# Performance work log

Measured on AMD Instinct MI355X. Metric: run time of the kernel, lower is better.

Reference implementation:

```python
import jax, jax.numpy as jnp
import numpy as np

B, L, D, H = 32, 1024, 512, 512
ODE_STEPS = 6
DT = 1.0

def _unif(key, shape, fan_in):
    bound = 1.0 / np.sqrt(fan_in)
    return jax.random.uniform(key, shape, jnp.float32, -bound, bound)

def setup_inputs() -> dict:
    key = jax.random.key(0)
    ks = jax.random.split(key, 9)
    return {
        "x": jax.random.normal(ks[0], (B, L, D), jnp.float32),
        "log_tau": jnp.zeros((H,), jnp.float32),
        "W_in": _unif(ks[1], (H, D), D),
        "b_in": _unif(ks[2], (H,), D),
        "W_rec": _unif(ks[3], (H, H), H),
        "W_gate": _unif(ks[4], (H, D + H), D + H),
        "b_gate": _unif(ks[5], (H,), D + H),
        "W_out": _unif(ks[6], (H, H), H),
        "b_out": _unif(ks[7], (H,), H),
    }

def reference(x, log_tau, W_in, b_in, W_rec, W_gate, b_gate, W_out, b_out):
    Bx, Lx, Dx = x.shape
    Hx = log_tau.shape[0]
    tau = jnp.exp(log_tau)                      # (H,)
    sub_dt = DT / ODE_STEPS
    # Split gate weight: cat([x, h]) @ W_gate.T == x @ Wg_x.T + h @ Wg_h.T
    Wg_x, Wg_h = W_gate[:, :Dx], W_gate[:, Dx:]
    # Precompute input-dependent drives for the whole sequence (time-parallel GEMMs)
    drive = jnp.einsum('bld,hd->blh', x, W_in) + b_in      # W_in(x), (B,L,H)
    gate_x = jnp.einsum('bld,hd->blh', x, Wg_x) + b_gate   # input part of gate pre-act

    def step(h, inp):
        d, gx = inp  # (B,H) each
        for _ in range(ODE_STEPS):  # small fixed unroll of ODE sub-steps
            rec = h @ W_rec.T
            gate = jax.nn.sigmoid(gx + h @ Wg_h.T)
            f = -h + gate * jnp.tanh(d + rec)
            h = h + (sub_dt / tau) * f
        return h, h

    h0 = jnp.zeros((Bx, Hx), x.dtype)
    h_last, fwd = jax.lax.scan(step, h0, (drive.transpose(1, 0, 2), gate_x.transpose(1, 0, 2)))
    fwd = fwd.transpose(1, 0, 2)                 # (B,L,H)
    output = fwd @ W_out.T + b_out               # output_proj; dropout is identity (p=0)
    return output, h_last
```

## Files before the change

kernel.cpp:

```cpp
#include <hip/hip_runtime.h>

typedef unsigned short u16;
typedef unsigned int   u32;
typedef unsigned long long u64;

#define LTC_B 32
#define LTC_L 1024
#define LTC_D 512
#define LTC_H 512
#define NG 8
#define NP 16
#define NBG 4

typedef _Float16 f16x8  __attribute__((ext_vector_type(8)));
typedef _Float16 f16x2t __attribute__((ext_vector_type(2)));
typedef float    f32x4  __attribute__((ext_vector_type(4)));

static __device__ __forceinline__ u32 packh(float a, float b) {
    f16x2t p; p[0] = (_Float16)a; p[1] = (_Float16)b;
    return __builtin_bit_cast(u32, p);
}
static __device__ __forceinline__ float unplo(u32 w) {
    return (float)__builtin_bit_cast(f16x2t, w)[0];
}
static __device__ __forceinline__ float unphi(u32 w) {
    return (float)__builtin_bit_cast(f16x2t, w)[1];
}
static __device__ __forceinline__ float sigm(float x) {
    return 1.f / (1.f + __expf(-x));
}
static __device__ __forceinline__ float tanh_f(float x) {
    float e = __expf(2.f * x);
    return 1.f - 2.f / (e + 1.f);
}
static __device__ __forceinline__ f16x8 cvt8(const float* p) {
    const float4 a = *(const float4*)p;
    const float4 b = *(const float4*)(p + 4);
    f16x8 r;
    r[0] = (_Float16)a.x; r[1] = (_Float16)a.y; r[2] = (_Float16)a.z; r[3] = (_Float16)a.w;
    r[4] = (_Float16)b.x; r[5] = (_Float16)b.y; r[6] = (_Float16)b.z; r[7] = (_Float16)b.w;
    return r;
}
static __device__ __forceinline__ bool stamp4(u64 a, u64 b, u64 c, u64 d, u32 k) {
    return ((u32)(a >> 32) == k) & ((u32)(b >> 32) == k) &
           ((u32)(c >> 32) == k) & ((u32)(d >> 32) == k);
}

__global__ __launch_bounds__(256) void gemm_a32_c16(
    const float* __restrict__ A, const float* __restrict__ W, int ldb,
    const float* __restrict__ bias, u16* __restrict__ C)
{
    const int wave = threadIdx.x >> 6;
    const int lane = threadIdx.x & 63;
    const int tile = blockIdx.x * 4 + wave;
    const int nt = tile & 7;
    const int mt = tile >> 3;
    const int r16 = lane & 15;
    const int kq  = (lane >> 4) * 8;

    const float* ap = A + (size_t)(mt * 64 + r16) * LTC_D + kq;
    const float* wp = W + (size_t)(nt * 64 + r16) * ldb + kq;

    f32x4 acc[4][4];
    #pragma unroll
    for (int i = 0; i < 4; ++i)
        #pragma unroll
        for (int jj = 0; jj < 4; ++jj) acc[i][jj] = (f32x4){0.f, 0.f, 0.f, 0.f};

    for (int ks = 0; ks < 16; ++ks) {
        f16x8 af[4], bf[4];
        #pragma unroll
        for (int t = 0; t < 4; ++t) {
            af[t] = cvt8(ap + (size_t)t * 16 * LTC_D + ks * 32);
            bf[t] = cvt8(wp + (size_t)t * 16 * ldb  + ks * 32);
        }
        #pragma unroll
        for (int mi = 0; mi < 4; ++mi)
            #pragma unroll
            for (int ni = 0; ni < 4; ++ni)
                acc[mi][ni] = __builtin_amdgcn_mfma_f32_16x16x32_f16(
                    af[mi], bf[ni], acc[mi][ni], 0, 0, 0);
    }
    const int row = (lane >> 4) * 4;
    const int col = lane & 15;
    #pragma unroll
    for (int ni = 0; ni < 4; ++ni) {
        const int n = nt * 64 + ni * 16 + col;
        const float bv = bias[n];
        #pragma unroll
        for (int mi = 0; mi < 4; ++mi)
            #pragma unroll
            for (int r = 0; r < 4; ++r) {
                _Float16 h = (_Float16)(acc[mi][ni][r] + bv);
                C[(size_t)(mt * 64 + mi * 16 + row + r) * LTC_H + n] =
                    __builtin_bit_cast(u16, h);
            }
    }
}

__global__ __launch_bounds__(256) void gemm_a16_c32(
    const u16* __restrict__ A, const float* __restrict__ W,
    const float* __restrict__ bias, float* __restrict__ C)
{
    const int wave = threadIdx.x >> 6;
    const int lane = threadIdx.x & 63;
    const int tile = blockIdx.x * 4 + wave;
    const int nt = tile & 7;
    const int mt = tile >> 3;
    const int r16 = lane & 15;
    const int kq  = (lane >> 4) * 8;

    const _Float16* ap = (const _Float16*)A + (size_t)(mt * 64 + r16) * LTC_D + kq;
    const float*    wp = W + (size_t)(nt * 64 + r16) * LTC_H + kq;

    f32x4 acc[4][4];
    #pragma unroll
    for (int i = 0; i < 4; ++i)
        #pragma unroll
        for (int jj = 0; jj < 4; ++jj) acc[i][jj] = (f32x4){0.f, 0.f, 0.f, 0.f};

    for (int ks = 0; ks < 16; ++ks) {
        f16x8 af[4], bf[4];
        #pragma unroll
        for (int t = 0; t < 4; ++t) {
            af[t] = *(const f16x8*)(ap + (size_t)t * 16 * LTC_D + ks * 32);
            bf[t] = cvt8(wp + (size_t)t * 16 * LTC_H + ks * 32);
        }
        #pragma unroll
        for (int mi = 0; mi < 4; ++mi)
            #pragma unroll
            for (int ni = 0; ni < 4; ++ni)
                acc[mi][ni] = __builtin_amdgcn_mfma_f32_16x16x32_f16(
                    af[mi], bf[ni], acc[mi][ni], 0, 0, 0);
    }
    const int row = (lane >> 4) * 4;
    const int col = lane & 15;
    #pragma unroll
    for (int ni = 0; ni < 4; ++ni) {
        const int n = nt * 64 + ni * 16 + col;
        const float bv = bias[n];
        #pragma unroll
        for (int mi = 0; mi < 4; ++mi)
            #pragma unroll
            for (int r = 0; r < 4; ++r)
                C[(size_t)(mt * 64 + mi * 16 + row + r) * LTC_H + n] =
                    acc[mi][ni][r] + bv;
    }
}

__global__ __launch_bounds__(256) void ltc_scan(
    u32* __restrict__ drive,
    const u32* __restrict__ gatex,
    const float* __restrict__ W_rec,
    const float* __restrict__ W_gate,
    const float* __restrict__ log_tau,
    u64* __restrict__ hbuf,
    float* __restrict__ hlast)
{
    const int g   = blockIdx.x & 7;
    const int p   = blockIdx.x >> 3;
    const int tid = threadIdx.x;
    const int lane = tid & 63;
    const int wv   = tid >> 6;

    __shared__ u32 hTu[16][260];
    __shared__ float red[64][17];

    const int nl = wv * 16 + (lane & 15);
    const int kq = (lane >> 4) * 8;
    const float* wrow = (nl < 32)
        ? (W_rec  + (size_t)(32 * p + nl) * LTC_H)
        : (W_gate + (size_t)(32 * p + nl - 32) * (LTC_D + LTC_H) + LTC_D);
    f16x8 Wf[16];
    #pragma unroll
    for (int ks = 0; ks < 16; ++ks) Wf[ks] = cvt8(wrow + ks * 32 + kq);

    for (int i = tid; i < 16 * 260; i += 256) (&hTu[0][0])[i] = 0;
    __syncthreads();

    const int ub = tid >> 4;
    const int jp = tid & 15;
    const int j0 = 32 * p + 2 * jp;
    const int gb = g * NBG + ub;
    float h0 = 0.f, h1 = 0.f, stau0 = 0.f, stau1 = 0.f;
    size_t dwofs = 0;
    if (tid < 64) {
        stau0 = (1.f / 6.f) * __expf(-log_tau[j0]);
        stau1 = (1.f / 6.f) * __expf(-log_tau[j0 + 1]);
        dwofs = (size_t)gb * LTC_L * 256 + 16 * p + jp;
    }

    const _Float16* hrow = (const _Float16*)&hTu[lane & 15][0];
    u32 kp1 = 0;
    int budget = 1 << 22;

    u32 dw = 0, gw = 0;
    if (tid < 64) { dw = drive[dwofs]; gw = gatex[dwofs]; }

    for (int l = 0; l < LTC_L; ++l) {
        const float d0 = unplo(dw), d1 = unphi(dw);
        const float gx0 = unplo(gw), gx1 = unphi(gw);
        u32 dn = 0, gn = 0;
        if (tid < 64 && l + 1 < LTC_L) {
            dn = drive[dwofs + (size_t)(l + 1) * 256];
            gn = gatex[dwofs + (size_t)(l + 1) * 256];
        }
        #pragma unroll 1
        for (int s = 0; s < 6; ++s) {
            f32x4 acc0 = (f32x4){0.f, 0.f, 0.f, 0.f}, acc1 = acc0;
            #pragma unroll
            for (int ks = 0; ks < 16; ks += 2) {
                const f16x8 a0 = *(const f16x8*)(hrow + ks * 32 + kq);
                const f16x8 a1 = *(const f16x8*)(hrow + (ks + 1) * 32 + kq);
                acc0 = __builtin_amdgcn_mfma_f32_16x16x32_f16(a0, Wf[ks],     acc0, 0, 0, 0);
                acc1 = __builtin_amdgcn_mfma_f32_16x16x32_f16(a1, Wf[ks + 1], acc1, 0, 0, 0);
            }
            {
                const int n  = wv * 16 + (lane & 15);
                const int rb = (lane >> 4) * 4;
                #pragma unroll
                for (int r = 0; r < 4; ++r) red[n][rb + r] = acc0[r] + acc1[r];
            }
            __syncthreads();
            ++kp1;
            const size_t pbase = (size_t)((kp1 & 1u) * NG + g) * (NBG * 256);
            if (tid < 64) {
                const float rec0 = red[2 * jp][ub],     gh0 = red[32 + 2 * jp][ub];
                const float rec1 = red[2 * jp + 1][ub], gh1 = red[32 + 2 * jp + 1][ub];
                h0 += stau0 * (sigm(gx0 + gh0) * tanh_f(d0 + rec0) - h0);
                h1 += stau1 * (sigm(gx1 + gh1) * tanh_f(d1 + rec1) - h1);
                const u64 v = ((u64)kp1 << 32) | (u64)packh(h0, h1);
                __hip_atomic_store(hbuf + pbase + (size_t)ub * 256 + 16 * p + jp,
                                   v, __ATOMIC_RELAXED, __HIP_MEMORY_SCOPE_AGENT);
            }
            {
                const u64* sb = hbuf + pbase + tid;
                u64 a0, a1, a2, a3;
                bool ok;
                do {
                    a0 = __hip_atomic_load(sb,       __ATOMIC_RELAXED,
                                           __HIP_MEMORY_SCOPE_AGENT);
                    a1 = __hip_atomic_load(sb + 256, __ATOMIC_RELAXED,
                                           __HIP_MEMORY_SCOPE_AGENT);
                    a2 = __hip_atomic_load(sb + 512, __ATOMIC_RELAXED,
                                           __HIP_MEMORY_SCOPE_AGENT);
                    a3 = __hip_atomic_load(sb + 768, __ATOMIC_RELAXED,
                                           __HIP_MEMORY_SCOPE_AGENT);
                    ok = stamp4(a0, a1, a2, a3, kp1);
                } while (!ok && --budget > 0);
                hTu[0][tid] = (u32)a0; hTu[1][tid] = (u32)a1;
                hTu[2][tid] = (u32)a2; hTu[3][tid] = (u32)a3;
            }
            __syncthreads();
        }
        if (tid < 64) drive[dwofs + (size_t)l * 256] = packh(h0, h1);
        dw = dn; gw = gn;
    }
    if (tid < 64) {
        hlast[(size_t)gb * LTC_H + j0]     = h0;
        hlast[(size_t)gb * LTC_H + j0 + 1] = h1;
    }
}

extern "C" void kernel_launch(void* const* d_in, const int* in_sizes, int n_in,
                              void* d_out, int out_size, void* d_ws, size_t ws_size,
                              hipStream_t stream)
{
    const float* x       = (const float*)d_in[0];
    const float* log_tau = (const float*)d_in[1];
    const float* W_in    = (const float*)d_in[2];
    const float* b_in    = (const float*)d_in[3];
    const float* W_rec   = (const float*)d_in[4];
    const float* W_gate  = (const float*)d_in[5];
    const float* b_gate  = (const float*)d_in[6];
    const float* W_out   = (const float*)d_in[7];
    const float* b_out   = (const float*)d_in[8];

    float* out   = (float*)d_out;
    float* hlast = out + (size_t)LTC_B * LTC_L * LTC_H;

    u32* ws    = (u32*)d_ws;
    u32* drive = ws;
    u32* gatex = ws + 8388608;
    u64* hbuf  = (u64*)(ws + 16777216);

    const int blocks = (LTC_B * LTC_L / 64) * (LTC_H / 64) / 4;

    gemm_a32_c16<<<blocks, 256, 0, stream>>>(x, W_in, LTC_D, b_in, (u16*)drive);
    gemm_a32_c16<<<blocks, 256, 0, stream>>>(x, W_gate, LTC_D + LTC_H, b_gate, (u16*)gatex);
    ltc_scan<<<NG * NP, 256, 0, stream>>>(drive, gatex, W_rec, W_gate, log_tau,
                                          hbuf, hlast);
    gemm_a16_c32<<<blocks, 256, 0, stream>>>((const u16*)drive, W_out, b_out, out);
}
```

Measured before the change: 10.81 ms.

## Pipeline recurrent scan per batch-row chunk to overlap polling with MFMA

```diff
diff --git a/kernel.cpp b/kernel.cpp
--- a/kernel.cpp
+++ b/kernel.cpp
@@ -40,10 +40,6 @@
     r[0] = (_Float16)a.x; r[1] = (_Float16)a.y; r[2] = (_Float16)a.z; r[3] = (_Float16)a.w;
     r[4] = (_Float16)b.x; r[5] = (_Float16)b.y; r[6] = (_Float16)b.z; r[7] = (_Float16)b.w;
     return r;
-}
-static __device__ __forceinline__ bool stamp4(u64 a, u64 b, u64 c, u64 d, u32 k) {
-    return ((u32)(a >> 32) == k) & ((u32)(b >> 32) == k) &
-           ((u32)(c >> 32) == k) & ((u32)(d >> 32) == k);
 }
 
 __global__ __launch_bounds__(256) void gemm_a32_c16(
@@ -164,7 +160,7 @@
     const int wv   = tid >> 6;
 
     __shared__ u32 hTu[16][260];
-    __shared__ float red[64][17];
+    __shared__ float redc[4][68];
 
     const int nl = wv * 16 + (lane & 15);
     const int kq = (lane >> 4) * 8;
@@ -207,51 +203,42 @@
         }
         #pragma unroll 1
         for (int s = 0; s < 6; ++s) {
-            f32x4 acc0 = (f32x4){0.f, 0.f, 0.f, 0.f}, acc1 = acc0;
-            #pragma unroll
-            for (int ks = 0; ks < 16; ks += 2) {
-                const f16x8 a0 = *(const f16x8*)(hrow + ks * 32 + kq);
-                const f16x8 a1 = *(const f16x8*)(hrow + (ks + 1) * 32 + kq);
-                acc0 = __builtin_amdgcn_mfma_f32_16x16x32_f16(a0, Wf[ks],     acc0, 0, 0, 0);
-                acc1 = __builtin_amdgcn_mfma_f32_16x16x32_f16(a1, Wf[ks + 1], acc1, 0, 0, 0);
+            ++kp1;
+            const u32 pk = kp1 - 1;
+            const size_t pubbase = (size_t)(((kp1 & 1u) * NG + g) * NBG) * 256;
+            const size_t polbase = (size_t)(((pk  & 1u) * NG + g) * NBG) * 256;
+            #pragma unroll
+            for (int c = 0; c < NBG; ++c) {
+                if (pk) {
+                    const u64* sb = hbuf + polbase + (size_t)c * 256 + tid;
+                    u64 v;
+                    do {
+                        v = __hip_atomic_load(sb, __ATOMIC_RELAXED,
+                                              __HIP_MEMORY_SCOPE_AGENT);
+                    } while ((u32)(v >> 32) != pk && --budget > 0);
+                    hTu[c][tid] = (u32)v;
+                }
+                __syncthreads();
+                f32x4 acc0 = (f32x4){0.f, 0.f, 0.f, 0.f}, acc1 = acc0;
+                #pragma unroll
+                for (int ks = 0; ks < 16; ks += 2) {
+                    const f16x8 a0 = *(const f16x8*)(hrow + ks * 32 + kq);
+                    const f16x8 a1 = *(const f16x8*)(hrow + (ks + 1) * 32 + kq);
+                    acc0 = __builtin_amdgcn_mfma_f32_16x16x32_f16(a0, Wf[ks],     acc0, 0, 0, 0);
+                    acc1 = __builtin_amdgcn_mfma_f32_16x16x32_f16(a1, Wf[ks + 1], acc1, 0, 0, 0);
+                }
+                if (lane < 16) redc[c][wv * 16 + lane] = acc0[c] + acc1[c];
+                __syncthreads();
+                if (tid < 64 && ub == c) {
+                    const float rec0 = redc[c][2 * jp],      gh0 = redc[c][32 + 2 * jp];
+                    const float rec1 = redc[c][2 * jp + 1],  gh1 = redc[c][33 + 2 * jp];
+                    h0 += stau0 * (sigm(gx0 + gh0) * tanh_f(d0 + rec0) - h0);
+                    h1 += stau1 * (sigm(gx1 + gh1) * tanh_f(d1 + rec1) - h1);
+                    const u64 v = ((u64)kp1 << 32) | (u64)packh(h0, h1);
+                    __hip_atomic_store(hbuf + pubbase + (size_t)c * 256 + 16 * p + jp,
+                                       v, __ATOMIC_RELAXED, __HIP_MEMORY_SCOPE_AGENT);
+                }
             }
-            {
-                const int n  = wv * 16 + (lane & 15);
-                const int rb = (lane >> 4) * 4;
-                #pragma unroll
-                for (int r = 0; r < 4; ++r) red[n][rb + r] = acc0[r] + acc1[r];
-            }
-            __syncthreads();
-            ++kp1;
-            const size_t pbase = (size_t)((kp1 & 1u) * NG + g) * (NBG * 256);
-            if (tid < 64) {
-                const float rec0 = red[2 * jp][ub],     gh0 = red[32 + 2 * jp][ub];
-                const float rec1 = red[2 * jp + 1][ub], gh1 = red[32 + 2 * jp + 1][ub];
-                h0 += stau0 * (sigm(gx0 + gh0) * tanh_f(d0 + rec0) - h0);
-                h1 += stau1 * (sigm(gx1 + gh1) * tanh_f(d1 + rec1) - h1);
-                const u64 v = ((u64)kp1 << 32) | (u64)packh(h0, h1);
-                __hip_atomic_store(hbuf + pbase + (size_t)ub * 256 + 16 * p + jp,
-                                   v, __ATOMIC_RELAXED, __HIP_MEMORY_SCOPE_AGENT);
-            }
-            {
-                const u64* sb = hbuf + pbase + tid;
-                u64 a0, a1, a2, a3;
-                bool ok;
-                do {
-                    a0 = __hip_atomic_load(sb,       __ATOMIC_RELAXED,
-                                           __HIP_MEMORY_SCOPE_AGENT);
-                    a1 = __hip_atomic_load(sb + 256, __ATOMIC_RELAXED,
-                                           __HIP_MEMORY_SCOPE_AGENT);
-                    a2 = __hip_atomic_load(sb + 512, __ATOMIC_RELAXED,
-                                           __HIP_MEMORY_SCOPE_AGENT);
-                    a3 = __hip_atomic_load(sb + 768, __ATOMIC_RELAXED,
-                                           __HIP_MEMORY_SCOPE_AGENT);
-                    ok = stamp4(a0, a1, a2, a3, kp1);
-                } while (!ok && --budget > 0);
-                hTu[0][tid] = (u32)a0; hTu[1][tid] = (u32)a1;
-                hTu[2][tid] = (u32)a2; hTu[3][tid] = (u32)a3;
-            }
-            __syncthreads();
         }
         if (tid < 64) drive[dwofs + (size_t)l * 256] = packh(h0, h1);
         dw = dn; gw = gn;
```

Result: slower. 22.05 ms (+104.0%).

## Add fast vectorized polling path for cross-block hidden-state exchange with safe fallback

Applied to the files above, without the earlier changes.

```diff
diff --git a/kernel.cpp b/kernel.cpp
--- a/kernel.cpp
+++ b/kernel.cpp
@@ -15,6 +15,7 @@
 typedef _Float16 f16x8  __attribute__((ext_vector_type(8)));
 typedef _Float16 f16x2t __attribute__((ext_vector_type(2)));
 typedef float    f32x4  __attribute__((ext_vector_type(4)));
+typedef unsigned int u32x4 __attribute__((ext_vector_type(4)));
 
 static __device__ __forceinline__ u32 packh(float a, float b) {
     f16x2t p; p[0] = (_Float16)a; p[1] = (_Float16)b;
@@ -44,6 +45,19 @@
 static __device__ __forceinline__ bool stamp4(u64 a, u64 b, u64 c, u64 d, u32 k) {
     return ((u32)(a >> 32) == k) & ((u32)(b >> 32) == k) &
            ((u32)(c >> 32) == k) & ((u32)(d >> 32) == k);
+}
+static __device__ __forceinline__ void ldfast32(const u64* p,
+        u64& a0, u64& a1, u64& a2, u64& a3) {
+    u32x4 r0, r1;
+    asm volatile(
+        "global_load_dwordx4 %0, %2, off sc0\n\t"
+        "global_load_dwordx4 %1, %3, off sc0\n\t"
+        "s_waitcnt vmcnt(0)"
+        : "=&v"(r0), "=&v"(r1)
+        : "v"(p), "v"(p + 2)
+        : "memory");
+    a0 = ((u64)r0.y << 32) | r0.x;  a1 = ((u64)r0.w << 32) | r0.z;
+    a2 = ((u64)r1.y << 32) | r1.x;  a3 = ((u64)r1.w << 32) | r1.z;
 }
 
 __global__ __launch_bounds__(256) void gemm_a32_c16(
@@ -154,7 +168,8 @@
     const float* __restrict__ W_rec,
     const float* __restrict__ W_gate,
     const float* __restrict__ log_tau,
-    u64* __restrict__ hbuf,
+    u64* __restrict__ hfast,
+    u64* __restrict__ hsafe,
     float* __restrict__ hlast)
 {
     const int g   = blockIdx.x & 7;
@@ -193,6 +208,7 @@
     const _Float16* hrow = (const _Float16*)&hTu[lane & 15][0];
     u32 kp1 = 0;
     int budget = 1 << 22;
+    int trust  = 4;
 
     u32 dw = 0, gw = 0;
     if (tid < 64) { dw = drive[dwofs]; gw = gatex[dwofs]; }
@@ -223,31 +239,45 @@
             }
             __syncthreads();
             ++kp1;
-            const size_t pbase = (size_t)((kp1 & 1u) * NG + g) * (NBG * 256);
+            const size_t pbase = (size_t)(((kp1 & 1u) * NG + g)) * (256 * NBG);
             if (tid < 64) {
                 const float rec0 = red[2 * jp][ub],     gh0 = red[32 + 2 * jp][ub];
                 const float rec1 = red[2 * jp + 1][ub], gh1 = red[32 + 2 * jp + 1][ub];
                 h0 += stau0 * (sigm(gx0 + gh0) * tanh_f(d0 + rec0) - h0);
                 h1 += stau1 * (sigm(gx1 + gh1) * tanh_f(d1 + rec1) - h1);
                 const u64 v = ((u64)kp1 << 32) | (u64)packh(h0, h1);
-                __hip_atomic_store(hbuf + pbase + (size_t)ub * 256 + 16 * p + jp,
-                                   v, __ATOMIC_RELAXED, __HIP_MEMORY_SCOPE_AGENT);
+                const size_t w = pbase + (size_t)(16 * p + jp) * NBG + ub;
+                *(volatile u64*)(hfast + w) = v;
+                __hip_atomic_store(hsafe + w, v, __ATOMIC_RELAXED,
+                                   __HIP_MEMORY_SCOPE_AGENT);
             }
             {
-                const u64* sb = hbuf + pbase + tid;
-                u64 a0, a1, a2, a3;
-                bool ok;
-                do {
-                    a0 = __hip_atomic_load(sb,       __ATOMIC_RELAXED,
-                                           __HIP_MEMORY_SCOPE_AGENT);
-                    a1 = __hip_atomic_load(sb + 256, __ATOMIC_RELAXED,
-                                           __HIP_MEMORY_SCOPE_AGENT);
-                    a2 = __hip_atomic_load(sb + 512, __ATOMIC_RELAXED,
-                                           __HIP_MEMORY_SCOPE_AGENT);
-                    a3 = __hip_atomic_load(sb + 768, __ATOMIC_RELAXED,
-                                           __HIP_MEMORY_SCOPE_AGENT);
-                    ok = stamp4(a0, a1, a2, a3, kp1);
-                } while (!ok && --budget > 0);
+                u64 a0 = 0, a1 = 0, a2 = 0, a3 = 0;
+                bool hit = false;
+                if (trust > 0) {
+                    const u64* fb = hfast + pbase + (size_t)tid * NBG;
+                    for (int it = 0; it < 8 && !hit; ++it) {
+                        ldfast32(fb, a0, a1, a2, a3);
+                        hit = stamp4(a0, a1, a2, a3, kp1);
+                    }
+                    trust = hit ? 4 : (trust - 1);
+                } else if ((kp1 & 63u) == 0u) {
+                    trust = 1;
+                }
+                if (!hit) {
+                    const u64* sb = hsafe + pbase + (size_t)tid * NBG;
+                    do {
+                        a0 = __hip_atomic_load(sb,     __ATOMIC_RELAXED,
+                                               __HIP_MEMORY_SCOPE_AGENT);
+                        a1 = __hip_atomic_load(sb + 1, __ATOMIC_RELAXED,
+                                               __HIP_MEMORY_SCOPE_AGENT);
+                        a2 = __hip_atomic_load(sb + 2, __ATOMIC_RELAXED,
+                                               __HIP_MEMORY_SCOPE_AGENT);
+                        a3 = __hip_atomic_load(sb + 3, __ATOMIC_RELAXED,
+                                               __HIP_MEMORY_SCOPE_AGENT);
+                        hit = stamp4(a0, a1, a2, a3, kp1);
+                    } while (!hit && --budget > 0);
+                }
                 hTu[0][tid] = (u32)a0; hTu[1][tid] = (u32)a1;
                 hTu[2][tid] = (u32)a2; hTu[3][tid] = (u32)a3;
             }
@@ -282,13 +312,14 @@
     u32* ws    = (u32*)d_ws;
     u32* drive = ws;
     u32* gatex = ws + 8388608;
-    u64* hbuf  = (u64*)(ws + 16777216);
+    u64* hfast = (u64*)(ws + 16777216);
+    u64* hsafe = hfast + 16384;
 
     const int blocks = (LTC_B * LTC_L / 64) * (LTC_H / 64) / 4;
 
     gemm_a32_c16<<<blocks, 256, 0, stream>>>(x, W_in, LTC_D, b_in, (u16*)drive);
     gemm_a32_c16<<<blocks, 256, 0, stream>>>(x, W_gate, LTC_D + LTC_H, b_gate, (u16*)gatex);
     ltc_scan<<<NG * NP, 256, 0, stream>>>(drive, gatex, W_rec, W_gate, log_tau,
-                                          hbuf, hlast);
+                                          hfast, hsafe, hlast);
     gemm_a16_c32<<<blocks, 256, 0, stream>>>((const u16*)drive, W_out, b_out, out);
 }
```

Result: slower. 17.00 ms (+57.2%).
